# Kernel optimization log

Measured on AMD Instinct MI355X. Metric: run time of the kernel, lower is better.

The kernel has to match this reference:

```python
import jax, jax.numpy as jnp
import numpy as np

N_NODES = 50000
N_EDGES = 800000
F_IN, F_HID, F_OUT = 128, 256, 256


def setup_inputs() -> dict:
    key = jax.random.key(0)
    ks = jax.random.split(key, 8)
    x = jax.random.normal(ks[0], (N_NODES, F_IN), dtype=jnp.float32)
    edge_index = jax.random.randint(ks[1], (2, N_EDGES), 0, N_NODES, dtype=jnp.int64)

    def lin(k, fan_in, fan_out):
        return jax.random.normal(k, (fan_in, fan_out), dtype=jnp.float32) / np.sqrt(fan_in).astype(np.float32)

    return {
        "x": x,
        "edge_index": edge_index,
        "W1": lin(ks[2], F_IN, F_HID),  "b1": jnp.zeros((F_HID,), jnp.float32),
        "W2": lin(ks[3], F_HID, F_HID), "b2": jnp.zeros((F_HID,), jnp.float32),
        "W3": lin(ks[4], F_HID, F_OUT), "b3": jnp.zeros((F_OUT,), jnp.float32),
    }


def reference(x, edge_index, W1, b1, W2, b2, W3, b3):
    # GCN (eval mode): edge_drop and feature dropout are identity; bn=False.
    n = x.shape[0]
    loops = jnp.arange(n, dtype=edge_index.dtype)
    src = jnp.concatenate([edge_index[0], loops])  # [E+N] with self-loops
    dst = jnp.concatenate([edge_index[1], loops])

    # Symmetric normalization deg^{-1/2}[src] * deg^{-1/2}[dst] (deg over dst incl. self-loops)
    deg = jax.ops.segment_sum(jnp.ones_like(dst, dtype=x.dtype), dst, num_segments=n)
    dinv = jnp.where(deg > 0, jax.lax.rsqrt(deg), jnp.zeros_like(deg))
    norm = dinv[src] * dinv[dst]  # [E+N]

    def gcn_conv(h, W, b):
        h = h @ W                                       # [N, out]
        msg = h[src] * norm[:, None]                    # gather + scale  [E+N, out]
        return jax.ops.segment_sum(msg, dst, num_segments=n) + b  # scatter-add

    h = jax.nn.relu(gcn_conv(x, W1, b1))
    h = jax.nn.relu(gcn_conv(h, W2, b2))
    return gcn_conv(h, W3, b3)
```

## Files before the change

### kernel.cpp

```cpp
#include <hip/hip_runtime.h>
#include <hip/hip_bf16.h>

#define NNODES 50000
#define NEDGES 800000
#define F_IN 128
#define F_HID 256

using u16 = unsigned short;
using f32x4 = __attribute__((ext_vector_type(4))) float;
using s16x8 = __attribute__((ext_vector_type(8))) short;

constexpr int SCAN_BLOCKS = (NNODES + 255) / 256;

constexpr size_t OFF_FLAG   = 0;
constexpr size_t OFF_DINV   = 256;
constexpr size_t OFF_ROWPTR = 200448;
constexpr size_t OFF_CNT    = 400640;
constexpr size_t OFF_BSUM   = 600832;
constexpr size_t OFF_BSUMS  = 601856;
constexpr size_t OFF_SRC    = 602880;
constexpr size_t OFF_DST    = 3802880;
constexpr size_t OFF_COL    = 7002880;
constexpr size_t OFF_NORM   = 10202880;
constexpr size_t OFF_XB     = 13402880;
constexpr size_t OFF_HB     = 26202880;
constexpr size_t OFF_AGGB   = 51802880;
constexpr size_t OFF_W1T    = 77402880;
constexpr size_t OFF_W2T    = 77468416;
constexpr size_t OFF_W3T    = 77599488;

static __device__ __forceinline__ float b2f(u16 u) {
    union { unsigned int i; float f; } v;
    v.i = ((unsigned int)u) << 16;
    return v.f;
}
static __device__ __forceinline__ u16 f2b(float f) {
    __hip_bfloat16 h = __float2bfloat16(f);
    return __builtin_bit_cast(u16, h);
}

__global__ void detect_kernel(const unsigned long long* __restrict__ p, int* __restrict__ flag) {
    __shared__ int bad;
    if (threadIdx.x == 0) bad = 0;
    __syncthreads();
    unsigned long long v = p[threadIdx.x];
    if (v >= (unsigned long long)NNODES) atomicAdd(&bad, 1);
    __syncthreads();
    if (threadIdx.x == 0) *flag = (bad == 0) ? 1 : 0;
}

__global__ __launch_bounds__(256) void convert_kernel(const void* __restrict__ raw,
                                                      const int* __restrict__ flag,
                                                      int* __restrict__ src, int* __restrict__ dst,
                                                      int* __restrict__ cnt) {
    int e = blockIdx.x * 256 + threadIdx.x;
    if (e >= NEDGES) return;
    int s, d;
    if (*flag) {
        const long long* p = (const long long*)raw;
        s = (int)p[e];
        d = (int)p[NEDGES + e];
    } else {
        const int* p = (const int*)raw;
        s = p[e];
        d = p[NEDGES + e];
    }
    src[e] = s;
    dst[e] = d;
    atomicAdd(&cnt[d], 1);
}

__global__ __launch_bounds__(256) void scan_reduce(const int* __restrict__ cnt, int* __restrict__ bsum,
                                                   float* __restrict__ dinv) {
    __shared__ int s[256];
    int i = blockIdx.x * 256 + threadIdx.x;
    int c = (i < NNODES) ? cnt[i] : 0;
    if (i < NNODES) dinv[i] = rsqrtf((float)c + 1.0f);
    s[threadIdx.x] = c;
    __syncthreads();
    for (int o = 128; o > 0; o >>= 1) {
        if (threadIdx.x < o) s[threadIdx.x] += s[threadIdx.x + o];
        __syncthreads();
    }
    if (threadIdx.x == 0) bsum[blockIdx.x] = s[0];
}

__global__ __launch_bounds__(256) void scan_top(const int* __restrict__ bsum, int* __restrict__ bsumS) {
    __shared__ int s[256];
    int t = threadIdx.x;
    int v = (t < SCAN_BLOCKS) ? bsum[t] : 0;
    s[t] = v;
    __syncthreads();
    for (int o = 1; o < 256; o <<= 1) {
        int tmp = (t >= o) ? s[t - o] : 0;
        __syncthreads();
        s[t] += tmp;
        __syncthreads();
    }
    if (t < SCAN_BLOCKS) bsumS[t] = s[t] - v;
}

__global__ __launch_bounds__(256) void scan_final(const int* __restrict__ cnt, const int* __restrict__ bsumS,
                                                  int* __restrict__ row_ptr) {
    __shared__ int s[256];
    int t = threadIdx.x;
    int i = blockIdx.x * 256 + t;
    int v = (i < NNODES) ? cnt[i] : 0;
    s[t] = v;
    __syncthreads();
    for (int o = 1; o < 256; o <<= 1) {
        int tmp = (t >= o) ? s[t - o] : 0;
        __syncthreads();
        s[t] += tmp;
        __syncthreads();
    }
    if (i < NNODES) row_ptr[i] = s[t] - v + bsumS[blockIdx.x];
    if (i == 0) row_ptr[NNODES] = NEDGES;
}

__global__ __launch_bounds__(256) void fill_kernel(const int* __restrict__ src, const int* __restrict__ dst,
                                                   const int* __restrict__ row_ptr, int* __restrict__ fillc,
                                                   const float* __restrict__ dinv,
                                                   int* __restrict__ col, float* __restrict__ normE) {
    int e = blockIdx.x * 256 + threadIdx.x;
    if (e >= NEDGES) return;
    int d = dst[e];
    int s = src[e];
    int p = row_ptr[d] + atomicAdd(&fillc[d], 1);
    col[p] = s;
    normE[p] = dinv[s] * dinv[d];
}

__global__ __launch_bounds__(256) void x2b_kernel(const float* __restrict__ x, u16* __restrict__ xb) {
    int i = blockIdx.x * 256 + threadIdx.x;
    float4 v = ((const float4*)x)[i];
    ushort4 o;
    o.x = f2b(v.x); o.y = f2b(v.y); o.z = f2b(v.z); o.w = f2b(v.w);
    ((ushort4*)xb)[i] = o;
}

__global__ __launch_bounds__(256) void wt_kernel(const float* __restrict__ W, u16* __restrict__ Wt, int K) {
    int idx = blockIdx.x * 256 + threadIdx.x;
    if (idx >= K * 256) return;
    int k = idx >> 8, n = idx & 255;
    Wt[n * K + k] = f2b(W[idx]);
}

template <int F>
__global__ __launch_bounds__(256) void agg_kernel(const u16* __restrict__ h,
                                                  const int* __restrict__ row_ptr,
                                                  const int* __restrict__ col,
                                                  const float* __restrict__ normE,
                                                  const float* __restrict__ dinv,
                                                  u16* __restrict__ outb) {
    constexpr int VEC = F / 64;
    int lane = threadIdx.x & 63;
    int v = __builtin_amdgcn_readfirstlane((int)(blockIdx.x * 4 + (threadIdx.x >> 6)));
    const size_t lo = (size_t)lane * VEC;

    float acc[VEC];
    float dv = dinv[v];
    {
        const u16* p = h + (size_t)v * F + lo;
        float w = dv * dv;
        if constexpr (VEC == 4) {
            ushort4 t = *(const ushort4*)p;
            acc[0] = w * b2f(t.x); acc[1] = w * b2f(t.y); acc[2] = w * b2f(t.z); acc[3] = w * b2f(t.w);
        } else {
            ushort2 t = *(const ushort2*)p;
            acc[0] = w * b2f(t.x); acc[1] = w * b2f(t.y);
        }
    }
    const int e0 = row_ptr[v], e1 = row_ptr[v + 1];
    for (int e = e0; e < e1; e += 8) {
        int   c[8];
        float w[8];
#pragma unroll
        for (int u = 0; u < 8; ++u) {
            int idx = e + u;
            int cl  = idx < e1 ? idx : e1 - 1;
            c[u] = col[cl];
            w[u] = idx < e1 ? normE[cl] : 0.0f;
        }
        if constexpr (VEC == 4) {
            ushort4 r[8];
#pragma unroll
            for (int u = 0; u < 8; ++u)
                r[u] = *(const ushort4*)(h + (size_t)c[u] * F + lo);
#pragma unroll
            for (int u = 0; u < 8; ++u) {
                acc[0] += w[u] * b2f(r[u].x);
                acc[1] += w[u] * b2f(r[u].y);
                acc[2] += w[u] * b2f(r[u].z);
                acc[3] += w[u] * b2f(r[u].w);
            }
        } else {
            ushort2 r[8];
#pragma unroll
            for (int u = 0; u < 8; ++u)
                r[u] = *(const ushort2*)(h + (size_t)c[u] * F + lo);
#pragma unroll
            for (int u = 0; u < 8; ++u) {
                acc[0] += w[u] * b2f(r[u].x);
                acc[1] += w[u] * b2f(r[u].y);
            }
        }
    }
    u16* o = outb + (size_t)v * F + lo;
    if constexpr (VEC == 4) {
        ushort4 t;
        t.x = f2b(acc[0]); t.y = f2b(acc[1]); t.z = f2b(acc[2]); t.w = f2b(acc[3]);
        *(ushort4*)o = t;
    } else {
        ushort2 t;
        t.x = f2b(acc[0]); t.y = f2b(acc[1]);
        *(ushort2*)o = t;
    }
}

template <int KT, bool RELU, bool OUT_BF16>
__global__ __launch_bounds__(256) void gemm_mfma(const u16* __restrict__ A, const u16* __restrict__ Wt,
                                                 const float* __restrict__ bias, void* __restrict__ outp,
                                                 int M) {
    constexpr int BM = 128, BN = 128, BK = 32;
    __shared__ __align__(16) u16 As[BM * BK];
    __shared__ __align__(16) u16 Bs[BN * BK];
    const int tid = threadIdx.x;
    const int lane = tid & 63, wid = tid >> 6;
    const int l15 = lane & 15, lhi = lane >> 4;
    const int m0 = blockIdx.x * BM, n0 = blockIdx.y * BN;
    const int wr = (wid >> 1) * 64, wc = (wid & 1) * 64;

    f32x4 acc[4][4] = {};

    const int sr = tid >> 1;
    const int sc2 = (tid & 1) * 2;

    for (int k0 = 0; k0 < KT; k0 += BK) {
        uint4 av0, av1, bv0, bv1;
        int ar = m0 + sr;
        if (ar < M) {
            const uint4* ap = (const uint4*)(A + (size_t)ar * KT + k0 + sc2 * 8);
            av0 = ap[0]; av1 = ap[1];
        } else {
            av0 = make_uint4(0, 0, 0, 0); av1 = av0;
        }
        const uint4* bp = (const uint4*)(Wt + (size_t)(n0 + sr) * KT + k0 + sc2 * 8);
        bv0 = bp[0]; bv1 = bp[1];

        __syncthreads();
        *(uint4*)&As[sr * BK + ((sc2 ^ (sr & 3)) * 8)]       = av0;
        *(uint4*)&As[sr * BK + (((sc2 + 1) ^ (sr & 3)) * 8)] = av1;
        *(uint4*)&Bs[sr * BK + ((sc2 ^ (sr & 3)) * 8)]       = bv0;
        *(uint4*)&Bs[sr * BK + (((sc2 + 1) ^ (sr & 3)) * 8)] = bv1;
        __syncthreads();

        s16x8 af[4], bfr[4];
#pragma unroll
        for (int m = 0; m < 4; ++m) {
            int r = wr + m * 16 + l15;
            af[m] = *(const s16x8*)&As[r * BK + ((lhi ^ (r & 3)) * 8)];
        }
#pragma unroll
        for (int n = 0; n < 4; ++n) {
            int r = wc + n * 16 + l15;
            bfr[n] = *(const s16x8*)&Bs[r * BK + ((lhi ^ (r & 3)) * 8)];
        }
#pragma unroll
        for (int m = 0; m < 4; ++m)
#pragma unroll
            for (int n = 0; n < 4; ++n)
                acc[m][n] = __builtin_amdgcn_mfma_f32_16x16x32_bf16(af[m], bfr[n], acc[m][n], 0, 0, 0);
    }

#pragma unroll
    for (int n = 0; n < 4; ++n) {
        int gcol = n0 + wc + n * 16 + l15;
        float bb = bias[gcol];
#pragma unroll
        for (int m = 0; m < 4; ++m) {
            int gr0 = m0 + wr + m * 16 + lhi * 4;
#pragma unroll
            for (int r = 0; r < 4; ++r) {
                int gr = gr0 + r;
                if (gr >= M) continue;
                float vv = acc[m][n][r] + bb;
                if (RELU) vv = vv > 0.f ? vv : 0.f;
                if (OUT_BF16)
                    ((u16*)outp)[(size_t)gr * 256 + gcol] = f2b(vv);
                else
                    ((float*)outp)[(size_t)gr * 256 + gcol] = vv;
            }
        }
    }
}

extern "C" void kernel_launch(void* const* d_in, const int* in_sizes, int n_in,
                              void* d_out, int out_size, void* d_ws, size_t ws_size,
                              hipStream_t stream) {
    const float* x  = (const float*)d_in[0];
    const void* edges = d_in[1];
    const float* W1 = (const float*)d_in[2];
    const float* b1 = (const float*)d_in[3];
    const float* W2 = (const float*)d_in[4];
    const float* b2 = (const float*)d_in[5];
    const float* W3 = (const float*)d_in[6];
    const float* b3 = (const float*)d_in[7];
    float* out = (float*)d_out;

    char* ws = (char*)d_ws;
    int*   flag   = (int*)(ws + OFF_FLAG);
    float* dinv   = (float*)(ws + OFF_DINV);
    int*   rowptr = (int*)(ws + OFF_ROWPTR);
    int*   cnt    = (int*)(ws + OFF_CNT);
    int*   bsum   = (int*)(ws + OFF_BSUM);
    int*   bsumS  = (int*)(ws + OFF_BSUMS);
    int*   src32  = (int*)(ws + OFF_SRC);
    int*   dst32  = (int*)(ws + OFF_DST);
    int*   col    = (int*)(ws + OFF_COL);
    float* normE  = (float*)(ws + OFF_NORM);
    u16*   xb     = (u16*)(ws + OFF_XB);
    u16*   hb     = (u16*)(ws + OFF_HB);
    u16*   aggb   = (u16*)(ws + OFF_AGGB);
    u16*   W1t    = (u16*)(ws + OFF_W1T);
    u16*   W2t    = (u16*)(ws + OFF_W2T);
    u16*   W3t    = (u16*)(ws + OFF_W3T);

    const int EB = (NEDGES + 255) / 256;

    hipMemsetAsync(cnt, 0, NNODES * sizeof(int), stream);
    detect_kernel<<<1, 256, 0, stream>>>((const unsigned long long*)edges, flag);
    convert_kernel<<<EB, 256, 0, stream>>>(edges, flag, src32, dst32, cnt);

    scan_reduce<<<SCAN_BLOCKS, 256, 0, stream>>>(cnt, bsum, dinv);
    scan_top<<<1, 256, 0, stream>>>(bsum, bsumS);
    scan_final<<<SCAN_BLOCKS, 256, 0, stream>>>(cnt, bsumS, rowptr);

    hipMemsetAsync(cnt, 0, NNODES * sizeof(int), stream);
    fill_kernel<<<EB, 256, 0, stream>>>(src32, dst32, rowptr, cnt, dinv, col, normE);

    x2b_kernel<<<(NNODES * F_IN / 4 + 255) / 256, 256, 0, stream>>>(x, xb);
    wt_kernel<<<(F_IN * 256 + 255) / 256, 256, 0, stream>>>(W1, W1t, F_IN);
    wt_kernel<<<(F_HID * 256 + 255) / 256, 256, 0, stream>>>(W2, W2t, F_HID);
    wt_kernel<<<(F_HID * 256 + 255) / 256, 256, 0, stream>>>(W3, W3t, F_HID);

    const int AGG_GRID = NNODES / 4;
    dim3 ggrid((NNODES + 127) / 128, 2);

    agg_kernel<F_IN><<<AGG_GRID, 256, 0, stream>>>(xb, rowptr, col, normE, dinv, aggb);
    gemm_mfma<F_IN, true, true><<<ggrid, 256, 0, stream>>>(aggb, W1t, b1, hb, NNODES);

    agg_kernel<F_HID><<<AGG_GRID, 256, 0, stream>>>(hb, rowptr, col, normE, dinv, aggb);
    gemm_mfma<F_HID, true, true><<<ggrid, 256, 0, stream>>>(aggb, W2t, b2, hb, NNODES);

    agg_kernel<F_HID><<<AGG_GRID, 256, 0, stream>>>(hb, rowptr, col, normE, dinv, aggb);
    gemm_mfma<F_HID, false, false><<<ggrid, 256, 0, stream>>>(aggb, W3t, b3, out, NNODES);
}
```

Measured before the change: 342.8 us.

## Build CSR via bucketed two-phase binning with 16-bit column indices

Replaces the per-edge global-atomic CSR fill with a two-phase build. Edges are first binned into 32-node buckets as packed (local dst, src) words, then each bucket is scattered with shared-memory atomics. Column indices shrink to 16 bits, and the per-edge norm array is dropped: the aggregator gathers dinv[src] and multiplies by dinv[dst] once at the end, which also removes the src/dst intermediate copies. The three weight-transpose launches are merged into one. The 16-bit packing relies on the node count fitting in 16 bits, and the aggregator now does a random dinv gather per edge in place of a streamed norm read.

```diff
diff --git a/kernel.cpp b/kernel.cpp
--- a/kernel.cpp
+++ b/kernel.cpp
@@ -7,10 +7,13 @@
 #define F_HID 256
 
 using u16 = unsigned short;
+using u32 = unsigned int;
 using f32x4 = __attribute__((ext_vector_type(4))) float;
 using s16x8 = __attribute__((ext_vector_type(8))) short;
 
 constexpr int SCAN_BLOCKS = (NNODES + 255) / 256;
+constexpr int BSHIFT = 5;
+constexpr int NBUCK = (NNODES + 31) >> 5;
 
 constexpr size_t OFF_FLAG   = 0;
 constexpr size_t OFF_DINV   = 256;
@@ -18,16 +21,15 @@
 constexpr size_t OFF_CNT    = 400640;
 constexpr size_t OFF_BSUM   = 600832;
 constexpr size_t OFF_BSUMS  = 601856;
-constexpr size_t OFF_SRC    = 602880;
-constexpr size_t OFF_DST    = 3802880;
-constexpr size_t OFF_COL    = 7002880;
-constexpr size_t OFF_NORM   = 10202880;
-constexpr size_t OFF_XB     = 13402880;
-constexpr size_t OFF_HB     = 26202880;
-constexpr size_t OFF_AGGB   = 51802880;
-constexpr size_t OFF_W1T    = 77402880;
-constexpr size_t OFF_W2T    = 77468416;
-constexpr size_t OFF_W3T    = 77599488;
+constexpr size_t OFF_BCUR   = 602880;
+constexpr size_t OFF_PAIRS  = 609280;
+constexpr size_t OFF_COL16  = 3809280;
+constexpr size_t OFF_XB     = 5409280;
+constexpr size_t OFF_HB     = 18209280;
+constexpr size_t OFF_AGGB   = 43809280;
+constexpr size_t OFF_W1T    = 69409280;
+constexpr size_t OFF_W2T    = 69474816;
+constexpr size_t OFF_W3T    = 69605888;
 
 static __device__ __forceinline__ float b2f(u16 u) {
     union { unsigned int i; float f; } v;
@@ -49,10 +51,72 @@
     if (threadIdx.x == 0) *flag = (bad == 0) ? 1 : 0;
 }
 
-__global__ __launch_bounds__(256) void convert_kernel(const void* __restrict__ raw,
-                                                      const int* __restrict__ flag,
-                                                      int* __restrict__ src, int* __restrict__ dst,
-                                                      int* __restrict__ cnt) {
+__global__ __launch_bounds__(256) void count_kernel(const void* __restrict__ raw,
+                                                    const int* __restrict__ flag,
+                                                    int* __restrict__ cnt) {
+    int e = blockIdx.x * 256 + threadIdx.x;
+    if (e >= NEDGES) return;
+    int d;
+    if (*flag) d = (int)((const long long*)raw)[NEDGES + e];
+    else       d = ((const int*)raw)[NEDGES + e];
+    atomicAdd(&cnt[d], 1);
+}
+
+__global__ __launch_bounds__(256) void scan_reduce(const int* __restrict__ cnt, int* __restrict__ bsum,
+                                                   float* __restrict__ dinv) {
+    __shared__ int s[256];
+    int i = blockIdx.x * 256 + threadIdx.x;
+    int c = (i < NNODES) ? cnt[i] : 0;
+    if (i < NNODES) dinv[i] = rsqrtf((float)c + 1.0f);
+    s[threadIdx.x] = c;
+    __syncthreads();
+    for (int o = 128; o > 0; o >>= 1) {
+        if (threadIdx.x < o) s[threadIdx.x] += s[threadIdx.x + o];
+        __syncthreads();
+    }
+    if (threadIdx.x == 0) bsum[blockIdx.x] = s[0];
+}
+
+__global__ __launch_bounds__(256) void scan_top(const int* __restrict__ bsum, int* __restrict__ bsumS) {
+    __shared__ int s[256];
+    int t = threadIdx.x;
+    int v = (t < SCAN_BLOCKS) ? bsum[t] : 0;
+    s[t] = v;
+    __syncthreads();
+    for (int o = 1; o < 256; o <<= 1) {
+        int tmp = (t >= o) ? s[t - o] : 0;
+        __syncthreads();
+        s[t] += tmp;
+        __syncthreads();
+    }
+    if (t < SCAN_BLOCKS) bsumS[t] = s[t] - v;
+}
+
+__global__ __launch_bounds__(256) void scan_final(const int* __restrict__ cnt, const int* __restrict__ bsumS,
+                                                  int* __restrict__ row_ptr, int* __restrict__ bcur) {
+    __shared__ int s[256];
+    int t = threadIdx.x;
+    int i = blockIdx.x * 256 + t;
+    int v = (i < NNODES) ? cnt[i] : 0;
+    s[t] = v;
+    __syncthreads();
+    for (int o = 1; o < 256; o <<= 1) {
+        int tmp = (t >= o) ? s[t - o] : 0;
+        __syncthreads();
+        s[t] += tmp;
+        __syncthreads();
+    }
+    if (i < NNODES) {
+        int rp = s[t] - v + bsumS[blockIdx.x];
+        row_ptr[i] = rp;
+        if ((i & 31) == 0) bcur[i >> BSHIFT] = rp;
+    }
+    if (i == 0) row_ptr[NNODES] = NEDGES;
+}
+
+__global__ __launch_bounds__(256) void phase1_bin(const void* __restrict__ raw,
+                                                  const int* __restrict__ flag,
+                                                  int* __restrict__ bcur, u32* __restrict__ pairs) {
     int e = blockIdx.x * 256 + threadIdx.x;
     if (e >= NEDGES) return;
     int s, d;
@@ -65,70 +129,34 @@
         s = p[e];
         d = p[NEDGES + e];
     }
-    src[e] = s;
-    dst[e] = d;
-    atomicAdd(&cnt[d], 1);
-}
-
-__global__ __launch_bounds__(256) void scan_reduce(const int* __restrict__ cnt, int* __restrict__ bsum,
-                                                   float* __restrict__ dinv) {
-    __shared__ int s[256];
-    int i = blockIdx.x * 256 + threadIdx.x;
-    int c = (i < NNODES) ? cnt[i] : 0;
-    if (i < NNODES) dinv[i] = rsqrtf((float)c + 1.0f);
-    s[threadIdx.x] = c;
-    __syncthreads();
-    for (int o = 128; o > 0; o >>= 1) {
-        if (threadIdx.x < o) s[threadIdx.x] += s[threadIdx.x + o];
-        __syncthreads();
-    }
-    if (threadIdx.x == 0) bsum[blockIdx.x] = s[0];
-}
-
-__global__ __launch_bounds__(256) void scan_top(const int* __restrict__ bsum, int* __restrict__ bsumS) {
-    __shared__ int s[256];
+    int pos = atomicAdd(&bcur[d >> BSHIFT], 1);
+    pairs[pos] = ((u32)(d & 31) << 16) | (u32)s;
+}
+
+__global__ __launch_bounds__(256) void phase2_fill(const u32* __restrict__ pairs,
+                                                   const int* __restrict__ row_ptr,
+                                                   u16* __restrict__ col) {
+    __shared__ int lcnt[32];
+    __shared__ int lbase[32];
+    int b = blockIdx.x;
+    int n0 = b << BSHIFT;
     int t = threadIdx.x;
-    int v = (t < SCAN_BLOCKS) ? bsum[t] : 0;
-    s[t] = v;
-    __syncthreads();
-    for (int o = 1; o < 256; o <<= 1) {
-        int tmp = (t >= o) ? s[t - o] : 0;
-        __syncthreads();
-        s[t] += tmp;
-        __syncthreads();
-    }
-    if (t < SCAN_BLOCKS) bsumS[t] = s[t] - v;
-}
-
-__global__ __launch_bounds__(256) void scan_final(const int* __restrict__ cnt, const int* __restrict__ bsumS,
-                                                  int* __restrict__ row_ptr) {
-    __shared__ int s[256];
-    int t = threadIdx.x;
-    int i = blockIdx.x * 256 + t;
-    int v = (i < NNODES) ? cnt[i] : 0;
-    s[t] = v;
-    __syncthreads();
-    for (int o = 1; o < 256; o <<= 1) {
-        int tmp = (t >= o) ? s[t - o] : 0;
-        __syncthreads();
-        s[t] += tmp;
-        __syncthreads();
-    }
-    if (i < NNODES) row_ptr[i] = s[t] - v + bsumS[blockIdx.x];
-    if (i == 0) row_ptr[NNODES] = NEDGES;
-}
-
-__global__ __launch_bounds__(256) void fill_kernel(const int* __restrict__ src, const int* __restrict__ dst,
-                                                   const int* __restrict__ row_ptr, int* __restrict__ fillc,
-                                                   const float* __restrict__ dinv,
-                                                   int* __restrict__ col, float* __restrict__ normE) {
-    int e = blockIdx.x * 256 + threadIdx.x;
-    if (e >= NEDGES) return;
-    int d = dst[e];
-    int s = src[e];
-    int p = row_ptr[d] + atomicAdd(&fillc[d], 1);
-    col[p] = s;
-    normE[p] = dinv[s] * dinv[d];
+    if (t < 32) {
+        lcnt[t] = 0;
+        int nd = n0 + t;
+        lbase[t] = (nd < NNODES) ? row_ptr[nd] : NEDGES;
+    }
+    __syncthreads();
+    int hi = n0 + 32; if (hi > NNODES) hi = NNODES;
+    int p0 = row_ptr[n0];
+    int p1 = row_ptr[hi];
+    for (int p = p0 + t; p < p1; p += 256) {
+        u32 pk = pairs[p];
+        int dl = (int)(pk >> 16);
+        int src = (int)(pk & 0xFFFFu);
+        int r = atomicAdd(&lcnt[dl], 1);
+        col[lbase[dl] + r] = (u16)src;
+    }
 }
 
 __global__ __launch_bounds__(256) void x2b_kernel(const float* __restrict__ x, u16* __restrict__ xb) {
@@ -139,18 +167,28 @@
     ((ushort4*)xb)[i] = o;
 }
 
-__global__ __launch_bounds__(256) void wt_kernel(const float* __restrict__ W, u16* __restrict__ Wt, int K) {
+__global__ __launch_bounds__(256) void wt_all(const float* __restrict__ W1, const float* __restrict__ W2,
+                                              const float* __restrict__ W3, u16* __restrict__ W1t,
+                                              u16* __restrict__ W2t, u16* __restrict__ W3t) {
     int idx = blockIdx.x * 256 + threadIdx.x;
-    if (idx >= K * 256) return;
-    int k = idx >> 8, n = idx & 255;
-    Wt[n * K + k] = f2b(W[idx]);
+    if (idx < 32768) {
+        int k = idx >> 8, n = idx & 255;
+        W1t[n * 128 + k] = f2b(W1[idx]);
+    } else if (idx < 98304) {
+        int j = idx - 32768;
+        int k = j >> 8, n = j & 255;
+        W2t[n * 256 + k] = f2b(W2[j]);
+    } else if (idx < 163840) {
+        int j = idx - 98304;
+        int k = j >> 8, n = j & 255;
+        W3t[n * 256 + k] = f2b(W3[j]);
+    }
 }
 
 template <int F>
 __global__ __launch_bounds__(256) void agg_kernel(const u16* __restrict__ h,
                                                   const int* __restrict__ row_ptr,
-                                                  const int* __restrict__ col,
-                                                  const float* __restrict__ normE,
+                                                  const u16* __restrict__ col,
                                                   const float* __restrict__ dinv,
                                                   u16* __restrict__ outb) {
     constexpr int VEC = F / 64;
@@ -162,13 +200,12 @@
     float dv = dinv[v];
     {
         const u16* p = h + (size_t)v * F + lo;
-        float w = dv * dv;
         if constexpr (VEC == 4) {
             ushort4 t = *(const ushort4*)p;
-            acc[0] = w * b2f(t.x); acc[1] = w * b2f(t.y); acc[2] = w * b2f(t.z); acc[3] = w * b2f(t.w);
+            acc[0] = dv * b2f(t.x); acc[1] = dv * b2f(t.y); acc[2] = dv * b2f(t.z); acc[3] = dv * b2f(t.w);
         } else {
             ushort2 t = *(const ushort2*)p;
-            acc[0] = w * b2f(t.x); acc[1] = w * b2f(t.y);
+            acc[0] = dv * b2f(t.x); acc[1] = dv * b2f(t.y);
         }
     }
     const int e0 = row_ptr[v], e1 = row_ptr[v + 1];
@@ -177,43 +214,50 @@
         float w[8];
 #pragma unroll
         for (int u = 0; u < 8; ++u) {
-            int idx = e + u;
-            int cl  = idx < e1 ? idx : e1 - 1;
-            c[u] = col[cl];
-            w[u] = idx < e1 ? normE[cl] : 0.0f;
+            if (e + u < e1) {
+                c[u] = (int)col[e + u];
+                w[u] = dinv[c[u]];
+            } else {
+                c[u] = 0;
+                w[u] = 0.0f;
+            }
         }
         if constexpr (VEC == 4) {
             ushort4 r[8];
 #pragma unroll
             for (int u = 0; u < 8; ++u)
-                r[u] = *(const ushort4*)(h + (size_t)c[u] * F + lo);
+                if (e + u < e1) r[u] = *(const ushort4*)(h + (size_t)c[u] * F + lo);
 #pragma unroll
             for (int u = 0; u < 8; ++u) {
-                acc[0] += w[u] * b2f(r[u].x);
-                acc[1] += w[u] * b2f(r[u].y);
-                acc[2] += w[u] * b2f(r[u].z);
-                acc[3] += w[u] * b2f(r[u].w);
+                if (e + u < e1) {
+                    acc[0] += w[u] * b2f(r[u].x);
+                    acc[1] += w[u] * b2f(r[u].y);
+                    acc[2] += w[u] * b2f(r[u].z);
+                    acc[3] += w[u] * b2f(r[u].w);
+                }
             }
         } else {
             ushort2 r[8];
 #pragma unroll
             for (int u = 0; u < 8; ++u)
-                r[u] = *(const ushort2*)(h + (size_t)c[u] * F + lo);
+                if (e + u < e1) r[u] = *(const ushort2*)(h + (size_t)c[u] * F + lo);
 #pragma unroll
             for (int u = 0; u < 8; ++u) {
-                acc[0] += w[u] * b2f(r[u].x);
-                acc[1] += w[u] * b2f(r[u].y);
+                if (e + u < e1) {
+                    acc[0] += w[u] * b2f(r[u].x);
+                    acc[1] += w[u] * b2f(r[u].y);
+                }
             }
         }
     }
     u16* o = outb + (size_t)v * F + lo;
     if constexpr (VEC == 4) {
         ushort4 t;
-        t.x = f2b(acc[0]); t.y = f2b(acc[1]); t.z = f2b(acc[2]); t.w = f2b(acc[3]);
+        t.x = f2b(dv * acc[0]); t.y = f2b(dv * acc[1]); t.z = f2b(dv * acc[2]); t.w = f2b(dv * acc[3]);
         *(ushort4*)o = t;
     } else {
         ushort2 t;
-        t.x = f2b(acc[0]); t.y = f2b(acc[1]);
+        t.x = f2b(dv * acc[0]); t.y = f2b(dv * acc[1]);
         *(ushort2*)o = t;
     }
 }
@@ -315,10 +359,9 @@
     int*   cnt    = (int*)(ws + OFF_CNT);
     int*   bsum   = (int*)(ws + OFF_BSUM);
     int*   bsumS  = (int*)(ws + OFF_BSUMS);
-    int*   src32  = (int*)(ws + OFF_SRC);
-    int*   dst32  = (int*)(ws + OFF_DST);
-    int*   col    = (int*)(ws + OFF_COL);
-    float* normE  = (float*)(ws + OFF_NORM);
+    int*   bcur   = (int*)(ws + OFF_BCUR);
+    u32*   pairs  = (u32*)(ws + OFF_PAIRS);
+    u16*   col16  = (u16*)(ws + OFF_COL16);
     u16*   xb     = (u16*)(ws + OFF_XB);
     u16*   hb     = (u16*)(ws + OFF_HB);
     u16*   aggb   = (u16*)(ws + OFF_AGGB);
@@ -330,29 +373,27 @@
 
     hipMemsetAsync(cnt, 0, NNODES * sizeof(int), stream);
     detect_kernel<<<1, 256, 0, stream>>>((const unsigned long long*)edges, flag);
-    convert_kernel<<<EB, 256, 0, stream>>>(edges, flag, src32, dst32, cnt);
+    count_kernel<<<EB, 256, 0, stream>>>(edges, flag, cnt);
 
     scan_reduce<<<SCAN_BLOCKS, 256, 0, stream>>>(cnt, bsum, dinv);
     scan_top<<<1, 256, 0, stream>>>(bsum, bsumS);
-    scan_final<<<SCAN_BLOCKS, 256, 0, stream>>>(cnt, bsumS, rowptr);
-
-    hipMemsetAsync(cnt, 0, NNODES * sizeof(int), stream);
-    fill_kernel<<<EB, 256, 0, stream>>>(src32, dst32, rowptr, cnt, dinv, col, normE);
+    scan_final<<<SCAN_BLOCKS, 256, 0, stream>>>(cnt, bsumS, rowptr, bcur);
+
+    phase1_bin<<<EB, 256, 0, stream>>>(edges, flag, bcur, pairs);
+    phase2_fill<<<NBUCK, 256, 0, stream>>>(pairs, rowptr, col16);
 
     x2b_kernel<<<(NNODES * F_IN / 4 + 255) / 256, 256, 0, stream>>>(x, xb);
-    wt_kernel<<<(F_IN * 256 + 255) / 256, 256, 0, stream>>>(W1, W1t, F_IN);
-    wt_kernel<<<(F_HID * 256 + 255) / 256, 256, 0, stream>>>(W2, W2t, F_HID);
-    wt_kernel<<<(F_HID * 256 + 255) / 256, 256, 0, stream>>>(W3, W3t, F_HID);
+    wt_all<<<640, 256, 0, stream>>>(W1, W2, W3, W1t, W2t, W3t);
 
     const int AGG_GRID = NNODES / 4;
     dim3 ggrid((NNODES + 127) / 128, 2);
 
-    agg_kernel<F_IN><<<AGG_GRID, 256, 0, stream>>>(xb, rowptr, col, normE, dinv, aggb);
+    agg_kernel<F_IN><<<AGG_GRID, 256, 0, stream>>>(xb, rowptr, col16, dinv, aggb);
     gemm_mfma<F_IN, true, true><<<ggrid, 256, 0, stream>>>(aggb, W1t, b1, hb, NNODES);
 
-    agg_kernel<F_HID><<<AGG_GRID, 256, 0, stream>>>(hb, rowptr, col, normE, dinv, aggb);
+    agg_kernel<F_HID><<<AGG_GRID, 256, 0, stream>>>(hb, rowptr, col16, dinv, aggb);
     gemm_mfma<F_HID, true, true><<<ggrid, 256, 0, stream>>>(aggb, W2t, b2, hb, NNODES);
 
-    agg_kernel<F_HID><<<AGG_GRID, 256, 0, stream>>>(hb, rowptr, col, normE, dinv, aggb);
+    agg_kernel<F_HID><<<AGG_GRID, 256, 0, stream>>>(hb, rowptr, col16, dinv, aggb);
     gemm_mfma<F_HID, false, false><<<ggrid, 256, 0, stream>>>(aggb, W3t, b3, out, NNODES);
 }
```

Result: slower. 465.4 us (+35.8%).
